# Performance work log

Measured on AMD Instinct MI355X. Metric: run time of the kernel, lower is better.

Reference implementation:

```python
import jax, jax.numpy as jnp
import numpy as np

TOP_K = 2
NEG_INF = -1.0e9


def setup_inputs() -> dict:
    key = jax.random.key(0)
    k = jax.random.split(key, 5)
    B, S, D, E = 4, 2048, 1024, 8
    H = 2 * D
    x = jax.random.normal(k[0], (B, S, D), dtype=jnp.float32)
    gate_w = jax.random.normal(k[1], (D, E), dtype=jnp.float32) * 0.02
    gate_b = jnp.zeros((E,), dtype=jnp.float32)
    w1 = jax.random.normal(k[2], (E, D, H), dtype=jnp.float32) * 0.02
    b1 = jnp.zeros((E, H), dtype=jnp.float32)
    w2 = jax.random.normal(k[3], (E, H, D), dtype=jnp.float32) * 0.02
    b2 = jnp.zeros((E, D), dtype=jnp.float32)
    noise = jax.random.normal(k[4], (B, S, E), dtype=jnp.float32)
    return {"x": x, "gate_w": gate_w, "gate_b": gate_b,
            "w1": w1, "b1": b1, "w2": w2, "b2": b2, "noise": noise}


def reference(x, gate_w, gate_b, w1, b1, w2, b2, noise):
    B, S, D = x.shape
    # Gating: linear + small gaussian noise (hk.next_rng_key equivalent)
    gating_logits = jnp.einsum('bsd,de->bse', x, gate_w) + gate_b + noise * 0.01
    # keep_top_k: mask all but top-k logits to -1e9
    top_k_values, top_k_indices = jax.lax.top_k(gating_logits, TOP_K)
    mask = gating_logits >= jnp.min(top_k_values, axis=-1, keepdims=True)
    gating_logits = jnp.where(mask, gating_logits, NEG_INF)
    gating_probs = jax.nn.softmax(gating_logits, axis=-1)
    # Dense compute of ALL experts on ALL tokens (as in source): [E,B,S,D]
    h = jax.nn.silu(jnp.einsum('bsd,edh->ebsh', x, w1) + b1[:, None, None, :])
    expert_outputs = jnp.einsum('ebsh,ehd->ebsd', h, w2) + b2[:, None, None, :]
    # Gather top-k expert outputs per token: [B,S,K,D]
    bi = jnp.arange(B)[:, None, None]
    si = jnp.arange(S)[None, :, None]
    selected = expert_outputs[top_k_indices, bi, si]
    top_k_gating_probs = jnp.take_along_axis(gating_probs, top_k_indices, axis=-1)
    final_output = jnp.einsum('bskd,bsk->bsd', selected, top_k_gating_probs)
    # Load-balancing aux loss on the MASKED logits (as in source)
    routing_probs = jax.nn.softmax(gating_logits, axis=-1)
    expert_usage = jnp.sum(routing_probs, axis=(0, 1))
    expert_importance = expert_usage / jnp.sum(expert_usage)
    mean_imp = jnp.mean(expert_importance)
    std_imp = jnp.std(expert_importance)
    aux_loss = std_imp / (mean_imp + 1e-10)
    return final_output, top_k_indices, aux_loss
```

## Files before the change

kernel.cpp:

```cpp
#include <hip/hip_runtime.h>
#include <stdint.h>


#define NTOK   8192
#define DIM    1024
#define NEXP   8
#define HID    2048
#define OUT_MAIN (NTOK * DIM)
#define IDX_OFF  OUT_MAIN
#define AUX_OFF  (OUT_MAIN + NTOK * 2)
#define MAXBLK 72

typedef __attribute__((ext_vector_type(8))) short short8;
typedef __attribute__((ext_vector_type(4))) float floatx4;

__device__ __forceinline__ unsigned short f2bf(float f) {
  unsigned int b = __float_as_uint(f);
  b += 0x7FFFu + ((b >> 16) & 1u);
  return (unsigned short)(b >> 16);
}

__global__ __launch_bounds__(1024) void k_gating(
    const float* __restrict__ x, const float* __restrict__ gate_w,
    const float* __restrict__ gate_b, const float* __restrict__ noise,
    float* __restrict__ out, int* __restrict__ counts,
    int* __restrict__ lists_tok, float* __restrict__ lists_p,
    float* __restrict__ probs_all, unsigned short* __restrict__ xb)
{
  const int lane = threadIdx.x & 63;
  const int wv   = threadIdx.x >> 6;
  const int t    = blockIdx.x * 16 + wv;
  const float* xr = x + (size_t)t * DIM;

  __shared__ int   cnt[NEXP];
  __shared__ int   base[NEXP];
  __shared__ int   s_e[32];
  __shared__ int   s_pos[32];
  __shared__ float s_p[32];
  if (threadIdx.x < NEXP) cnt[threadIdx.x] = 0;

  double acc[NEXP] = {0,0,0,0,0,0,0,0};
  #pragma unroll
  for (int jj = 0; jj < 4; ++jj) {
    const int d0 = lane * 4 + jj * 256;
    const float4 xv = *(const float4*)(xr + d0);
    const float xs[4] = {xv.x, xv.y, xv.z, xv.w};
    unsigned short xbq[4];
    #pragma unroll
    for (int c = 0; c < 4; ++c) {
      const float4 g0 = *(const float4*)(gate_w + (size_t)(d0 + c) * NEXP);
      const float4 g1 = *(const float4*)(gate_w + (size_t)(d0 + c) * NEXP + 4);
      const double xd = (double)xs[c];
      acc[0] += xd * (double)g0.x; acc[1] += xd * (double)g0.y;
      acc[2] += xd * (double)g0.z; acc[3] += xd * (double)g0.w;
      acc[4] += xd * (double)g1.x; acc[5] += xd * (double)g1.y;
      acc[6] += xd * (double)g1.z; acc[7] += xd * (double)g1.w;
      xbq[c] = f2bf(xs[c]);
    }
    ushort4 q; q.x = xbq[0]; q.y = xbq[1]; q.z = xbq[2]; q.w = xbq[3];
    *(ushort4*)(xb + (size_t)t * DIM + d0) = q;
  }
  #pragma unroll
  for (int e = 0; e < NEXP; ++e) {
    #pragma unroll
    for (int off = 32; off; off >>= 1) acc[e] += __shfl_xor(acc[e], off);
  }
  __syncthreads();
  if (lane == 0) {
    double l[NEXP];
    #pragma unroll
    for (int e = 0; e < NEXP; ++e)
      l[e] = acc[e] + (double)gate_b[e] + 0.01 * (double)noise[(size_t)t * NEXP + e];
    int i1 = 0; double v1 = l[0];
    #pragma unroll
    for (int e = 1; e < NEXP; ++e) if (l[e] > v1) { v1 = l[e]; i1 = e; }
    int i2 = (i1 == 0) ? 1 : 0; double v2 = l[i2];
    #pragma unroll
    for (int e = 0; e < NEXP; ++e) if (e != i1 && l[e] > v2) { v2 = l[e]; i2 = e; }
    float pr[NEXP]; float Z = 0.f;
    #pragma unroll
    for (int e = 0; e < NEXP; ++e) {
      const float a = (l[e] >= v2) ? (float)(l[e] - v1) : -1.0e9f;
      pr[e] = __expf(a); Z += pr[e];
    }
    const float rz = 1.0f / Z;
    #pragma unroll
    for (int e = 0; e < NEXP; ++e) {
      pr[e] *= rz;
      probs_all[(size_t)t * NEXP + e] = pr[e];
    }
    out[(size_t)IDX_OFF + t * 2]     = (float)i1;
    out[(size_t)IDX_OFF + t * 2 + 1] = (float)i2;
    const int p1 = atomicAdd(&cnt[i1], 1);
    const int p2 = atomicAdd(&cnt[i2], 1);
    s_e[wv * 2]     = i1; s_pos[wv * 2]     = p1; s_p[wv * 2]     = pr[i1];
    s_e[wv * 2 + 1] = i2; s_pos[wv * 2 + 1] = p2; s_p[wv * 2 + 1] = pr[i2];
  }
  __syncthreads();
  if (threadIdx.x < NEXP) base[threadIdx.x] = atomicAdd(&counts[threadIdx.x], cnt[threadIdx.x]);
  __syncthreads();
  if (lane == 0) {
    #pragma unroll
    for (int k = 0; k < 2; ++k) {
      const int ee  = s_e[wv * 2 + k];
      const int pos = base[ee] + s_pos[wv * 2 + k];
      lists_tok[ee * NTOK + pos] = t;
      lists_p[ee * NTOK + pos]   = s_p[wv * 2 + k];
    }
  }
}

__global__ void k_offs(const int* __restrict__ counts, int* __restrict__ offs,
                       int* __restrict__ tbl_e, int* __restrict__ tbl_m,
                       int* __restrict__ nblk) {
  if (threadIdx.x == 0) {
    int a = 0;
    #pragma unroll
    for (int e = 0; e < NEXP; ++e) { offs[e] = a; a += counts[e]; }
    offs[NEXP] = a;
    int nb = 0;
    for (int e = 0; e < NEXP; ++e) {
      const int nbe = (counts[e] + 255) >> 8;
      for (int m = 0; m < nbe; ++m) { tbl_e[nb] = e; tbl_m[nb] = m << 8; ++nb; }
    }
    nblk[0] = nb;
    for (int b = nb; b < MAXBLK; ++b) { tbl_e[b] = 0; tbl_m[b] = 0; }
  }
}

__global__ __launch_bounds__(256) void k_aux(const float* __restrict__ probs_all,
                                             float* __restrict__ out) {
  float p[NEXP] = {0,0,0,0,0,0,0,0};
  for (int t = threadIdx.x; t < NTOK; t += 256) {
    const float4 a = *(const float4*)(probs_all + (size_t)t * NEXP);
    const float4 b = *(const float4*)(probs_all + (size_t)t * NEXP + 4);
    p[0] += a.x; p[1] += a.y; p[2] += a.z; p[3] += a.w;
    p[4] += b.x; p[5] += b.y; p[6] += b.z; p[7] += b.w;
  }
  #pragma unroll
  for (int e = 0; e < NEXP; ++e) {
    #pragma unroll
    for (int off = 32; off; off >>= 1) p[e] += __shfl_xor(p[e], off);
  }
  __shared__ float red[4][NEXP];
  const int lane = threadIdx.x & 63, wv = threadIdx.x >> 6;
  if (lane == 0) {
    #pragma unroll
    for (int e = 0; e < NEXP; ++e) red[wv][e] = p[e];
  }
  __syncthreads();
  if (threadIdx.x == 0) {
    float usage[NEXP], s = 0.f;
    #pragma unroll
    for (int e = 0; e < NEXP; ++e) {
      usage[e] = red[0][e] + red[1][e] + red[2][e] + red[3][e];
      s += usage[e];
    }
    float imp[NEXP], mean = 0.f, var = 0.f;
    #pragma unroll
    for (int e = 0; e < NEXP; ++e) { imp[e] = usage[e] / s; mean += imp[e]; }
    mean *= 0.125f;
    #pragma unroll
    for (int e = 0; e < NEXP; ++e) { const float d = imp[e] - mean; var += d * d; }
    var *= 0.125f;
    out[AUX_OFF] = sqrtf(var) / (mean + 1e-10f);
  }
}

__global__ __launch_bounds__(256) void k_tr(
    const float* __restrict__ in, unsigned short* __restrict__ out,
    int in_ld, size_t in_estride, int r0, int c0,
    int out_ld, size_t out_estride)
{
  const int e  = blockIdx.z;
  const int tr = blockIdx.x << 6;
  const int tc = blockIdx.y << 6;
  const int tid = threadIdx.x;
  __shared__ float t[64][65];
  const float* src = in + (size_t)e * in_estride + (size_t)(r0 + tr) * in_ld + (c0 + tc);
  #pragma unroll
  for (int p = 0; p < 4; ++p) {
    const int r  = (p << 4) + (tid >> 4);
    const int c4 = (tid & 15) << 2;
    const float4 v = *(const float4*)(src + (size_t)r * in_ld + c4);
    t[r][c4] = v.x; t[r][c4 + 1] = v.y; t[r][c4 + 2] = v.z; t[r][c4 + 3] = v.w;
  }
  __syncthreads();
  unsigned short* dst = out + (size_t)e * out_estride + (size_t)tc * out_ld + tr;
  #pragma unroll
  for (int p = 0; p < 4; ++p) {
    const int c  = (p << 4) + (tid >> 4);
    const int r4 = (tid & 15) << 2;
    ushort4 q;
    q.x = f2bf(t[r4][c]);     q.y = f2bf(t[r4 + 1][c]);
    q.z = f2bf(t[r4 + 2][c]); q.w = f2bf(t[r4 + 3][c]);
    *(ushort4*)(dst + (size_t)c * out_ld + r4) = q;
  }
}

template <int MODE>
__global__ __launch_bounds__(1024) void k_gemm(
    const unsigned short* __restrict__ Abase,
    const unsigned short* __restrict__ Bt,
    const float* __restrict__ bias,
    const int* __restrict__ counts, const int* __restrict__ offs,
    const int* __restrict__ tbl_e, const int* __restrict__ tbl_m,
    const int* __restrict__ nblk,
    const int* __restrict__ lists_tok, const float* __restrict__ lists_p,
    unsigned short* __restrict__ hout, float* __restrict__ out,
    const int hb, const int Hs)
{
  if ((int)blockIdx.x >= nblk[0]) return;
  const int e   = tbl_e[blockIdx.x];
  const int m0  = tbl_m[blockIdx.x];
  const int n_e = counts[e];

  int nb, k0g, Kloc;
  if (MODE == 0) { nb = blockIdx.y << 8; k0g = 0; Kloc = DIM; }
  else { nb = (blockIdx.y >> 1) << 8; const int half = Hs >> 1;
         k0g = (blockIdx.y & 1) * half; Kloc = half; }

  const int tid  = threadIdx.x;
  const int lane = tid & 63;
  const int wv   = tid >> 6;
  const int wm   = (wv & 3) << 6;
  const int wn   = (wv >> 2) << 6;

  __shared__ __align__(16) unsigned short as[2][256 * 32];
  __shared__ __align__(16) unsigned short bs[2][256 * 32];

  const int K = (MODE == 0) ? DIM : Hs;
  const unsigned short* Bexp = Bt + (size_t)e * ((size_t)DIM * Hs) + (size_t)nb * K + k0g;

  const int swk   = (((lane & 3) ^ ((lane >> 2) & 3)) << 3);
  const int rbase = wv << 4;
  const int r     = rbase + (lane >> 2);
  const int rcA   = (m0 + r < n_e) ? (m0 + r) : (n_e - 1);
  size_t arow;
  if (MODE == 0) arow = (size_t)lists_tok[e * NTOK + rcA] * DIM;
  else           arow = (size_t)(offs[e] + rcA) * Hs;
  const unsigned short* gpa = Abase + arow + k0g + swk;
  const unsigned short* gpb = Bexp + (size_t)r * K + swk;
  unsigned short* lpa0 = &as[0][rbase << 5];
  unsigned short* lpb0 = &bs[0][rbase << 5];
  unsigned short* lpa1 = &as[1][rbase << 5];
  unsigned short* lpb1 = &bs[1][rbase << 5];

  floatx4 acc[4][4];
  #pragma unroll
  for (int i = 0; i < 4; ++i)
    #pragma unroll
    for (int j = 0; j < 4; ++j) acc[i][j] = (floatx4){0.f, 0.f, 0.f, 0.f};

  auto issue = [&](int buf, int kko) {
    __builtin_amdgcn_global_load_lds(
        (const __attribute__((address_space(1))) void*)(gpa + kko),
        (__attribute__((address_space(3))) void*)(void*)(buf ? lpa1 : lpa0), 16, 0, 0);
    __builtin_amdgcn_global_load_lds(
        (const __attribute__((address_space(1))) void*)(gpb + kko),
        (__attribute__((address_space(3))) void*)(void*)(buf ? lpb1 : lpb0), 16, 0, 0);
  };

  issue(0, 0);
  int p = 0;
  for (int kk = 0; kk < Kloc; kk += 32) {
    __syncthreads();
    if (kk + 32 < Kloc) issue(p ^ 1, kk + 32);
    const int c = lane >> 4;
    short8 af[4];
    #pragma unroll
    for (int i = 0; i < 4; ++i) {
      const int row = wm + (i << 4) + (lane & 15);
      af[i] = *(const short8*)(&as[p][(row << 5) + ((c ^ (row & 3)) << 3)]);
    }
    short8 bfr[4];
    #pragma unroll
    for (int j = 0; j < 4; ++j) {
      const int row = wn + (j << 4) + (lane & 15);
      bfr[j] = *(const short8*)(&bs[p][(row << 5) + ((c ^ (row & 3)) << 3)]);
    }
    #pragma unroll
    for (int i = 0; i < 4; ++i)
      #pragma unroll
      for (int j = 0; j < 4; ++j)
        acc[i][j] = __builtin_amdgcn_mfma_f32_16x16x32_bf16(af[i], bfr[j], acc[i][j], 0, 0, 0);
    p ^= 1;
  }

  const int q4 = (lane >> 4) << 2;
  if (MODE == 0) {
    #pragma unroll
    for (int i = 0; i < 4; ++i) {
      #pragma unroll
      for (int j = 0; j < 4; ++j) {
        const int nloc = wn + (j << 4) + (lane & 15);
        const float bb = bias[e * HID + hb + nb + nloc];
        #pragma unroll
        for (int rr = 0; rr < 4; ++rr) {
          const int m = m0 + wm + (i << 4) + q4 + rr;
          if (m < n_e) {
            float v = acc[i][j][rr] + bb;
            v = v / (1.0f + __expf(-v));
            hout[(size_t)(offs[e] + m) * Hs + nb + nloc] = f2bf(v);
          }
        }
      }
    }
  } else {
    #pragma unroll
    for (int i = 0; i < 4; ++i) {
      #pragma unroll
      for (int rr = 0; rr < 4; ++rr) {
        const int m = m0 + wm + (i << 4) + q4 + rr;
        if (m < n_e) {
          const int   tok = lists_tok[e * NTOK + m];
          const float pp  = lists_p[e * NTOK + m];
          #pragma unroll
          for (int j = 0; j < 4; ++j) {
            const int d = nb + wn + (j << 4) + (lane & 15);
            float v = acc[i][j][rr];
            if (hb == 0 && k0g == 0) v += bias[e * DIM + d];
            atomicAdd(out + (size_t)tok * DIM + d, pp * v);
          }
        }
      }
    }
  }
}

extern "C" void kernel_launch(void* const* d_in, const int* in_sizes, int n_in,
                              void* d_out, int out_size, void* d_ws, size_t ws_size,
                              hipStream_t stream)
{
  const float* x      = (const float*)d_in[0];
  const float* gate_w = (const float*)d_in[1];
  const float* gate_b = (const float*)d_in[2];
  const float* w1     = (const float*)d_in[3];
  const float* b1     = (const float*)d_in[4];
  const float* w2     = (const float*)d_in[5];
  const float* b2     = (const float*)d_in[6];
  const float* noise  = (const float*)d_in[7];
  float* out = (float*)d_out;

  char* ws = (char*)d_ws;
  const size_t CNT_OFF = 0;
  const size_t OFF_OFF = 64;
  const size_t NBK_OFF = 128;
  const size_t TBE_OFF = 192;
  const size_t TBM_OFF = 1024;
  const size_t LT_OFF  = 2048;
  const size_t LP_OFF  = LT_OFF + 262144;
  const size_t PA_OFF  = LP_OFF + 262144;
  const size_t XB_OFF  = 1048576;
  const size_t W_OFF   = 17825792;

  int nsl = 0;
  for (int cand = 1; cand <= 8; cand <<= 1) {
    const size_t need = W_OFF + (size_t)(33554432 + 67108864) / (size_t)cand;
    if (ws_size >= need) { nsl = cand; break; }
  }
  if (!nsl) return;
  const int Hs = HID / nsl;

  int* counts          = (int*)(ws + CNT_OFF);
  int* offs            = (int*)(ws + OFF_OFF);
  int* nblk            = (int*)(ws + NBK_OFF);
  int* tbl_e           = (int*)(ws + TBE_OFF);
  int* tbl_m           = (int*)(ws + TBM_OFF);
  int* lists_tok       = (int*)(ws + LT_OFF);
  float* lists_p       = (float*)(ws + LP_OFF);
  float* probs_all     = (float*)(ws + PA_OFF);
  unsigned short* xb   = (unsigned short*)(ws + XB_OFF);
  unsigned short* wt   = (unsigned short*)(ws + W_OFF);
  unsigned short* hbuf = (unsigned short*)(ws + W_OFF + (size_t)33554432 / nsl);

  hipMemsetAsync(d_out, 0, (size_t)OUT_MAIN * sizeof(float), stream);
  hipMemsetAsync(ws + CNT_OFF, 0, 64, stream);

  k_gating<<<NTOK / 16, 1024, 0, stream>>>(x, gate_w, gate_b, noise, out, counts,
                                           lists_tok, lists_p, probs_all, xb);
  k_offs<<<1, 64, 0, stream>>>(counts, offs, tbl_e, tbl_m, nblk);
  k_aux<<<1, 256, 0, stream>>>(probs_all, out);

  for (int s = 0; s < nsl; ++s) {
    const int hb = s * Hs;
    dim3 gt1(DIM / 64, Hs / 64, NEXP);
    k_tr<<<gt1, 256, 0, stream>>>(w1, wt, HID, (size_t)DIM * HID, 0, hb,
                                  DIM, (size_t)Hs * DIM);
    dim3 g1(MAXBLK, Hs / 256, 1);
    k_gemm<0><<<g1, 1024, 0, stream>>>(xb, wt, b1, counts, offs, tbl_e, tbl_m, nblk,
                                       lists_tok, lists_p, hbuf, out, hb, Hs);
    dim3 gt2(Hs / 64, DIM / 64, NEXP);
    k_tr<<<gt2, 256, 0, stream>>>(w2, wt, DIM, (size_t)DIM * HID, hb, 0,
                                  Hs, (size_t)DIM * Hs);
    dim3 g2(MAXBLK, (DIM / 256) * 2, 1);
    k_gemm<1><<<g2, 1024, 0, stream>>>(hbuf, wt, b2, counts, offs, tbl_e, tbl_m, nblk,
                                       lists_tok, lists_p, hbuf, out, hb, Hs);
  }
}
```

Before: 404.1 us.

## Triple-buffer GEMM LDS pipeline with vmcnt waits and remap block order

The GEMM main loop moves from a double-buffered LDS pipeline with __syncthreads to a three-stage ring. Two tiles are prefetched ahead, and each iteration waits with explicit s_waitcnt vmcnt and a raw s_barrier, so global loads overlap more MFMA work. Block indices are also remapped from the linear id so that consecutive blocks are spread across tbl entries in an XCD-aware pattern, aiming for better L2 reuse of expert weights. The cost is 50% more shared memory per block, and the remap assumes gridDim.x is divisible by 8.

```diff
diff --git a/kernel.cpp b/kernel.cpp
--- a/kernel.cpp
+++ b/kernel.cpp
@@ -210,15 +210,20 @@
     unsigned short* __restrict__ hout, float* __restrict__ out,
     const int hb, const int Hs)
 {
-  if ((int)blockIdx.x >= nblk[0]) return;
-  const int e   = tbl_e[blockIdx.x];
-  const int m0  = tbl_m[blockIdx.x];
+  const int lin = blockIdx.y * gridDim.x + blockIdx.x;
+  const int q   = gridDim.x >> 3;
+  const int j   = lin >> 3;
+  const int bx  = (lin & 7) * q + j / gridDim.y;
+  const int by  = j % gridDim.y;
+  if (bx >= nblk[0]) return;
+  const int e   = tbl_e[bx];
+  const int m0  = tbl_m[bx];
   const int n_e = counts[e];
 
   int nb, k0g, Kloc;
-  if (MODE == 0) { nb = blockIdx.y << 8; k0g = 0; Kloc = DIM; }
-  else { nb = (blockIdx.y >> 1) << 8; const int half = Hs >> 1;
-         k0g = (blockIdx.y & 1) * half; Kloc = half; }
+  if (MODE == 0) { nb = by << 8; k0g = 0; Kloc = DIM; }
+  else { nb = (by >> 1) << 8; const int half = Hs >> 1;
+         k0g = (by & 1) * half; Kloc = half; }
 
   const int tid  = threadIdx.x;
   const int lane = tid & 63;
@@ -226,8 +231,8 @@
   const int wm   = (wv & 3) << 6;
   const int wn   = (wv >> 2) << 6;
 
-  __shared__ __align__(16) unsigned short as[2][256 * 32];
-  __shared__ __align__(16) unsigned short bs[2][256 * 32];
+  __shared__ __align__(16) unsigned short as[3][256 * 32];
+  __shared__ __align__(16) unsigned short bs[3][256 * 32];
 
   const int K = (MODE == 0) ? DIM : Hs;
   const unsigned short* Bexp = Bt + (size_t)e * ((size_t)DIM * Hs) + (size_t)nb * K + k0g;
@@ -241,50 +246,58 @@
   else           arow = (size_t)(offs[e] + rcA) * Hs;
   const unsigned short* gpa = Abase + arow + k0g + swk;
   const unsigned short* gpb = Bexp + (size_t)r * K + swk;
-  unsigned short* lpa0 = &as[0][rbase << 5];
-  unsigned short* lpb0 = &bs[0][rbase << 5];
-  unsigned short* lpa1 = &as[1][rbase << 5];
-  unsigned short* lpb1 = &bs[1][rbase << 5];
 
   floatx4 acc[4][4];
   #pragma unroll
   for (int i = 0; i < 4; ++i)
     #pragma unroll
-    for (int j = 0; j < 4; ++j) acc[i][j] = (floatx4){0.f, 0.f, 0.f, 0.f};
+    for (int j2 = 0; j2 < 4; ++j2) acc[i][j2] = (floatx4){0.f, 0.f, 0.f, 0.f};
 
   auto issue = [&](int buf, int kko) {
+    unsigned short* la = &as[buf][rbase << 5];
+    unsigned short* lb = &bs[buf][rbase << 5];
     __builtin_amdgcn_global_load_lds(
         (const __attribute__((address_space(1))) void*)(gpa + kko),
-        (__attribute__((address_space(3))) void*)(void*)(buf ? lpa1 : lpa0), 16, 0, 0);
+        (__attribute__((address_space(3))) void*)(void*)la, 16, 0, 0);
     __builtin_amdgcn_global_load_lds(
         (const __attribute__((address_space(1))) void*)(gpb + kko),
-        (__attribute__((address_space(3))) void*)(void*)(buf ? lpb1 : lpb0), 16, 0, 0);
+        (__attribute__((address_space(3))) void*)(void*)lb, 16, 0, 0);
   };
 
   issue(0, 0);
+  issue(1, 32);
   int p = 0;
   for (int kk = 0; kk < Kloc; kk += 32) {
-    __syncthreads();
-    if (kk + 32 < Kloc) issue(p ^ 1, kk + 32);
+    if (kk + 32 < Kloc) { asm volatile("s_waitcnt vmcnt(2)" ::: "memory"); }
+    else                { asm volatile("s_waitcnt vmcnt(0)" ::: "memory"); }
+    __builtin_amdgcn_sched_barrier(0);
+    __builtin_amdgcn_s_barrier();
+    __builtin_amdgcn_sched_barrier(0);
+    if (kk + 64 < Kloc) {
+      int ib = p - 1; if (ib < 0) ib = 2;
+      issue(ib, kk + 64);
+    }
+    const unsigned short* ap = &as[p][0];
+    const unsigned short* bp = &bs[p][0];
     const int c = lane >> 4;
     short8 af[4];
     #pragma unroll
     for (int i = 0; i < 4; ++i) {
       const int row = wm + (i << 4) + (lane & 15);
-      af[i] = *(const short8*)(&as[p][(row << 5) + ((c ^ (row & 3)) << 3)]);
+      af[i] = *(const short8*)(ap + (row << 5) + ((c ^ (row & 3)) << 3));
     }
     short8 bfr[4];
     #pragma unroll
-    for (int j = 0; j < 4; ++j) {
-      const int row = wn + (j << 4) + (lane & 15);
-      bfr[j] = *(const short8*)(&bs[p][(row << 5) + ((c ^ (row & 3)) << 3)]);
+    for (int j2 = 0; j2 < 4; ++j2) {
+      const int row = wn + (j2 << 4) + (lane & 15);
+      bfr[j2] = *(const short8*)(bp + (row << 5) + ((c ^ (row & 3)) << 3));
     }
     #pragma unroll
     for (int i = 0; i < 4; ++i)
       #pragma unroll
-      for (int j = 0; j < 4; ++j)
-        acc[i][j] = __builtin_amdgcn_mfma_f32_16x16x32_bf16(af[i], bfr[j], acc[i][j], 0, 0, 0);
-    p ^= 1;
+      for (int j2 = 0; j2 < 4; ++j2)
+        acc[i][j2] = __builtin_amdgcn_mfma_f32_16x16x32_bf16(af[i], bfr[j2], acc[i][j2], 0, 0, 0);
+    p = (p == 2) ? 0 : p + 1;
   }
 
   const int q4 = (lane >> 4) << 2;
@@ -292,14 +305,14 @@
     #pragma unroll
     for (int i = 0; i < 4; ++i) {
       #pragma unroll
-      for (int j = 0; j < 4; ++j) {
-        const int nloc = wn + (j << 4) + (lane & 15);
+      for (int j2 = 0; j2 < 4; ++j2) {
+        const int nloc = wn + (j2 << 4) + (lane & 15);
         const float bb = bias[e * HID + hb + nb + nloc];
         #pragma unroll
         for (int rr = 0; rr < 4; ++rr) {
           const int m = m0 + wm + (i << 4) + q4 + rr;
           if (m < n_e) {
-            float v = acc[i][j][rr] + bb;
+            float v = acc[i][j2][rr] + bb;
             v = v / (1.0f + __expf(-v));
             hout[(size_t)(offs[e] + m) * Hs + nb + nloc] = f2bf(v);
           }
@@ -316,9 +329,9 @@
           const int   tok = lists_tok[e * NTOK + m];
           const float pp  = lists_p[e * NTOK + m];
           #pragma unroll
-          for (int j = 0; j < 4; ++j) {
-            const int d = nb + wn + (j << 4) + (lane & 15);
-            float v = acc[i][j][rr];
+          for (int j2 = 0; j2 < 4; ++j2) {
+            const int d = nb + wn + (j2 << 4) + (lane & 15);
+            float v = acc[i][j2][rr];
             if (hb == 0 && k0g == 0) v += bias[e * DIM + d];
             atomicAdd(out + (size_t)tok * DIM + d, pp * v);
           }
```

New measurement: 466.8 us. 1.16x slower.
